# Optimization experiments

Measured on AMD Instinct MI355X. Metric: run time of the kernel, lower is better.

## Reference

```python
import jax, jax.numpy as jnp
import numpy as np

D = 1024
H = 16
HD = D // H  # 64
BASE = 10000.0


def _rope_tables(seq_len, dtype=jnp.float32):
    # inv_freq over even dims, rotate-half convention: emb = cat(freqs, freqs)
    inv_freq = 1.0 / (BASE ** (jnp.arange(0, HD, 2, dtype=jnp.float32) / HD))
    t = jnp.arange(seq_len, dtype=jnp.float32)
    freqs = jnp.einsum('i,j->ij', t, inv_freq)          # [S, HD/2]
    emb = jnp.concatenate([freqs, freqs], axis=-1)       # [S, HD]
    return jnp.cos(emb).astype(dtype), jnp.sin(emb).astype(dtype)


def _rotate_half(x):
    x1, x2 = jnp.split(x, 2, axis=-1)
    return jnp.concatenate([-x2, x1], axis=-1)


def setup_inputs() -> dict:
    key = jax.random.key(0)
    ks = jax.random.split(key, 5)
    B, S = 2, 2048
    scale = 0.02
    return {
        'x': jax.random.normal(ks[0], (B, S, D), dtype=jnp.float32),
        'wq': jax.random.normal(ks[1], (D, D), dtype=jnp.float32) * scale,
        'wk': jax.random.normal(ks[2], (D, D), dtype=jnp.float32) * scale,
        'wv': jax.random.normal(ks[3], (D, D), dtype=jnp.float32) * scale,
        'wo': jax.random.normal(ks[4], (D, D), dtype=jnp.float32) * scale,
    }


def reference(x, wq, wk, wv, wo):
    B, S, _ = x.shape
    # QKV projections (torch Linear: x @ W^T), split into heads -> [B, H, S, HD]
    def proj(w):
        return jnp.einsum('bsd,ed->bse', x, w).reshape(B, S, H, HD).transpose(0, 2, 1, 3)
    q, k, v = proj(wq), proj(wk), proj(wv)

    # RoPE (rotate-half)
    cos, sin = _rope_tables(S, x.dtype)                  # [S, HD]
    cos = cos[None, None, :, :]
    sin = sin[None, None, :, :]
    q = q * cos + _rotate_half(q) * sin
    k = k * cos + _rotate_half(k) * sin

    # causal scaled-dot-product attention
    scores = jnp.einsum('bhqd,bhkd->bhqk', q, k) / jnp.sqrt(jnp.array(HD, x.dtype))
    causal = jnp.tril(jnp.ones((S, S), dtype=bool))
    scores = jnp.where(causal[None, None], scores, jnp.finfo(x.dtype).min)
    attn = jax.nn.softmax(scores, axis=-1)
    out = jnp.einsum('bhqk,bhkd->bhqd', attn, v)         # [B, H, S, HD]

    out = out.transpose(0, 2, 1, 3).reshape(B, S, D)
    return jnp.einsum('bsd,ed->bse', out, wo)
```

## Files before the change

kernel.cpp:

```cpp
#include <hip/hip_runtime.h>
#include <cstdint>
#include <cstddef>

typedef unsigned short u16;
typedef unsigned int u32;
typedef __bf16 bf16x8 __attribute__((ext_vector_type(8)));
typedef float f32x4 __attribute__((ext_vector_type(4)));
typedef u16 u16x8 __attribute__((ext_vector_type(8)));
typedef u16 u16x4 __attribute__((ext_vector_type(4)));

#define DD 1024
#define HH 16
#define HDIM 64
#define BB 2
#define SS 2048
#define NQT 32

__device__ __forceinline__ u16 cvt(float f) {
  __bf16 h = (__bf16)f;
  return __builtin_bit_cast(u16, h);
}
__device__ __forceinline__ f32x4 mfma16(bf16x8 a, bf16x8 b, f32x4 c) {
  return __builtin_amdgcn_mfma_f32_16x16x32_bf16(a, b, c, 0, 0, 0);
}
__device__ __forceinline__ bf16x8 ld_bf8(const u16* p) {
  return __builtin_bit_cast(bf16x8, *(const u16x8*)p);
}
__device__ __forceinline__ void async16(const void* g, void* l) {
  __builtin_amdgcn_global_load_lds(
      (__attribute__((address_space(1))) void*)(uintptr_t)g,
      (__attribute__((address_space(3))) void*)l, 16, 0, 0);
}

__global__ void cast_all(const float* __restrict__ x, const float* __restrict__ wq,
                         const float* __restrict__ wk, const float* __restrict__ wv,
                         const float* __restrict__ wo, u16* __restrict__ xb,
                         u16* __restrict__ wqb, u16* __restrict__ wkb,
                         u16* __restrict__ wvb, u16* __restrict__ wob) {
  int i = blockIdx.x * 256 + threadIdx.x;
  const float* src;
  u16* dst;
  int off;
  if (i < (1 << 20)) {
    src = x; dst = xb; off = i;
  } else {
    int j = i - (1 << 20);
    int w = j >> 18;
    off = j & ((1 << 18) - 1);
    src = (w == 0) ? wq : (w == 1) ? wk : (w == 2) ? wv : wo;
    dst = (w == 0) ? wqb : (w == 1) ? wkb : (w == 2) ? wvb : wob;
  }
  float4 v = ((const float4*)src)[off];
  u16x4 o;
  o[0] = cvt(v.x); o[1] = cvt(v.y); o[2] = cvt(v.z); o[3] = cvt(v.w);
  *(u16x4*)&dst[(size_t)off * 4] = o;
}

__global__ __launch_bounds__(256) void gemm_qkv(
    const u16* __restrict__ xb, const u16* __restrict__ wq,
    const u16* __restrict__ wk, const u16* __restrict__ wv,
    u16* __restrict__ Qo, u16* __restrict__ Ko, u16* __restrict__ Vto) {
  __shared__ __align__(16) u16 As[2][128 * 32];
  __shared__ __align__(16) u16 Bs[2][128 * 32];
  const int t = threadIdx.x;
  const int w = t >> 6, l = t & 63, lane16 = l & 15, quad = l >> 4;
  const int m0 = blockIdx.x * 128, n0 = blockIdx.y * 128;
  const u16* wsel = (blockIdx.z == 0) ? wq : (blockIdx.z == 1) ? wk : wv;
  const int m_w = (w >> 1) * 64, n_w = (w & 1) * 64;
  const int srow = t >> 2, scol = (t & 3) * 8;
  const u16* a0 = &xb[(size_t)(m0 + srow) * DD + scol];
  const u16* a1 = &xb[(size_t)(m0 + 64 + srow) * DD + scol];
  const u16* b0 = &wsel[(size_t)(n0 + srow) * DD + scol];
  const u16* b1 = &wsel[(size_t)(n0 + 64 + srow) * DD + scol];

  async16(a0, &As[0][t * 8]);  async16(a1, &As[0][2048 + t * 8]);
  async16(b0, &Bs[0][t * 8]);  async16(b1, &Bs[0][2048 + t * 8]);

  f32x4 acc[4][4] = {};
  for (int kt = 0; kt < 32; ++kt) {
    __syncthreads();
    if (kt < 31) {
      const int nb = (kt + 1) & 1, ko = (kt + 1) * 32;
      async16(a0 + ko, &As[nb][t * 8]);
      async16(a1 + ko, &As[nb][2048 + t * 8]);
      async16(b0 + ko, &Bs[nb][t * 8]);
      async16(b1 + ko, &Bs[nb][2048 + t * 8]);
    }
    const u16* Ac = As[kt & 1];
    const u16* Bc = Bs[kt & 1];
    bf16x8 af[4], bfr[4];
#pragma unroll
    for (int mi = 0; mi < 4; ++mi)
      af[mi] = ld_bf8(&Ac[(m_w + mi * 16 + lane16) * 32 + quad * 8]);
#pragma unroll
    for (int ni = 0; ni < 4; ++ni)
      bfr[ni] = ld_bf8(&Bc[(n_w + ni * 16 + lane16) * 32 + quad * 8]);
#pragma unroll
    for (int mi = 0; mi < 4; ++mi)
#pragma unroll
      for (int ni = 0; ni < 4; ++ni)
        acc[mi][ni] = mfma16(af[mi], bfr[ni], acc[mi][ni]);
  }
  if (blockIdx.z == 2) {
#pragma unroll
    for (int mi = 0; mi < 4; ++mi) {
      int mbase = m0 + m_w + mi * 16 + quad * 4;
      int b = mbase >> 11, s0 = mbase & (SS - 1);
#pragma unroll
      for (int ni = 0; ni < 4; ++ni) {
        int e = n0 + n_w + ni * 16 + lane16;
        int h = e >> 6, d = e & 63;
        u16x4 pk;
#pragma unroll
        for (int r = 0; r < 4; ++r) pk[r] = cvt(acc[mi][ni][r]);
        *(u16x4*)&Vto[((size_t)(b * HH + h) * HDIM + d) * SS + s0] = pk;
      }
    }
  } else {
    u16* osel = (blockIdx.z == 0) ? Qo : Ko;
    const float scale = (blockIdx.z == 0) ? 0.18033688f : 1.0f;
    float invf[2];
    invf[0] = exp2f((float)lane16 * -0.4152410119f) * 0.15915494309f;
    invf[1] = exp2f((float)(16 + lane16) * -0.4152410119f) * 0.15915494309f;
    const int h = (n0 + n_w) >> 6;
#pragma unroll
    for (int mi = 0; mi < 4; ++mi) {
#pragma unroll
      for (int r = 0; r < 4; ++r) {
        int mrow = m0 + m_w + mi * 16 + quad * 4 + r;
        int b = mrow >> 11, s = mrow & (SS - 1);
        size_t rowbase = ((size_t)(b * HH + h) * SS + s) * HDIM;
#pragma unroll
        for (int ni = 0; ni < 2; ++ni) {
          float x1 = acc[mi][ni][r], x2 = acc[mi][ni + 2][r];
          float rv = (float)s * invf[ni];
          rv = rv - floorf(rv);
          float sn = __builtin_amdgcn_sinf(rv);
          float c  = __builtin_amdgcn_cosf(rv);
          int d = ni * 16 + lane16;
          osel[rowbase + d]      = cvt((x1 * c - x2 * sn) * scale);
          osel[rowbase + d + 32] = cvt((x2 * c + x1 * sn) * scale);
        }
      }
    }
  }
}

__global__ __launch_bounds__(256, 4) void attn_k(const u16* __restrict__ Qb,
                                                 const u16* __restrict__ Kb,
                                                 const u16* __restrict__ Vt,
                                                 u16* __restrict__ AO) {
  __shared__ __align__(16) u16 KsF[2][64 * 64];
  __shared__ __align__(16) u16 VtL[2][64 * 64];
  __shared__ __align__(16) u16 Ps[4][16 * 64];
  const int t = threadIdx.x;
  const int w = t >> 6, l = t & 63, lane16 = l & 15, quad = l >> 4;
  const int bh = blockIdx.x;
  const int jj = NQT - 1 - (int)blockIdx.y;
  const size_t base = (size_t)bh * SS * HDIM;
  const u16* Qp = Qb + base;
  const int b = bh >> 4, h = bh & 15;

  const int q0 = jj * 64;
  const int qrow = q0 + w * 16 + lane16;
  bf16x8 qf0 = ld_bf8(&Qp[(size_t)qrow * 64 + quad * 8]);
  bf16x8 qf1 = ld_bf8(&Qp[(size_t)qrow * 64 + 32 + quad * 8]);

  u16x8 onesu;
#pragma unroll
  for (int i = 0; i < 8; ++i) onesu[i] = 0x3F80;
  const bf16x8 ones = __builtin_bit_cast(bf16x8, onesu);

  f32x4 o[4] = {};
  f32x4 lacc = {};
  const f32x4 zf = {};

  const u16* kptr[2];
  const u16* vptr[2];
#pragma unroll
  for (int i = 0; i < 2; ++i) {
    int p = i * 256 + t;
    int r = p >> 3;
    int c = (p & 7) ^ (r & 7);
    kptr[i] = Kb + base + (size_t)r * 64 + c * 8;
    int d = p >> 3;
    int q = (p & 7) ^ (d & 7);
    vptr[i] = Vt + base + (size_t)d * SS + q * 8;
  }

#pragma unroll
  for (int i = 0; i < 2; ++i) {
    async16(kptr[i], &KsF[0][(i * 256 + t) * 8]);
    kptr[i] += 64 * 64;
    async16(vptr[i], &VtL[0][(i * 256 + t) * 8]);
    vptr[i] += 64;
  }

  u16* Pw = Ps[w];
  const int ktmax = jj;
  for (int kt = 0; kt <= ktmax; ++kt) {
    __syncthreads();
    if (kt < ktmax) {
      const int nb = (kt + 1) & 1;
#pragma unroll
      for (int i = 0; i < 2; ++i) {
        async16(kptr[i], &KsF[nb][(i * 256 + t) * 8]);
        kptr[i] += 64 * 64;
        async16(vptr[i], &VtL[nb][(i * 256 + t) * 8]);
        vptr[i] += 64;
      }
    }
    const u16* Kc = KsF[kt & 1];
    const u16* Vc = VtL[kt & 1];
    const int kv0 = kt * 64;
    f32x4 st[4];
    __builtin_amdgcn_s_setprio(1);
#pragma unroll
    for (int nc = 0; nc < 4; ++nc) {
      int rr = nc * 16 + lane16;
      int p0 = rr * 8 + (quad ^ (rr & 7));
      int p1 = rr * 8 + ((4 + quad) ^ (rr & 7));
      f32x4 a = mfma16(ld_bf8(&Kc[p0 * 8]), qf0, zf);
      a = mfma16(ld_bf8(&Kc[p1 * 8]), qf1, a);
      st[nc] = a;
    }
    __builtin_amdgcn_s_setprio(0);
    if (kt == ktmax) {
#pragma unroll
      for (int nc = 0; nc < 4; ++nc) {
        int kvb = kv0 + nc * 16 + quad * 4;
#pragma unroll
        for (int r = 0; r < 4; ++r)
          if (kvb + r > qrow) st[nc][r] = -3.0e38f;
      }
    }
#pragma unroll
    for (int nc = 0; nc < 4; ++nc)
#pragma unroll
      for (int r = 0; r < 4; ++r) st[nc][r] = __builtin_amdgcn_exp2f(st[nc][r]);
#pragma unroll
    for (int nc = 0; nc < 4; ++nc) {
      u16x4 pk;
#pragma unroll
      for (int r = 0; r < 4; ++r) pk[r] = cvt(st[nc][r]);
      int addr = lane16 * 64 + (((nc * 2 + (quad >> 1)) ^ (lane16 & 7)) * 8) + (quad & 1) * 4;
      *(u16x4*)&Pw[addr] = pk;
    }
    __builtin_amdgcn_s_setprio(1);
#pragma unroll
    for (int G = 0; G < 2; ++G) {
      int gc = ((G * 4 + quad) ^ (lane16 & 7)) * 8;
      bf16x8 pf = ld_bf8(&Pw[lane16 * 64 + gc]);
      lacc = mfma16(ones, pf, lacc);
#pragma unroll
      for (int nd = 0; nd < 4; ++nd) {
        int d = nd * 16 + lane16;
        bf16x8 bv = ld_bf8(&Vc[(size_t)d * 64 + gc]);
        o[nd] = mfma16(bv, pf, o[nd]);
      }
    }
    __builtin_amdgcn_s_setprio(0);
  }
  const float inv = 1.0f / lacc[0];
  const size_t rowb = (size_t)(b * SS + qrow) * DD + h * HDIM + quad * 4;
#pragma unroll
  for (int nd = 0; nd < 4; ++nd) {
    u16x4 pk;
#pragma unroll
    for (int r = 0; r < 4; ++r) pk[r] = cvt(o[nd][r] * inv);
    *(u16x4*)&AO[rowb + nd * 16] = pk;
  }
}

__global__ __launch_bounds__(256) void gemm_out(const u16* __restrict__ A, const u16* __restrict__ W,
                                                float* __restrict__ out) {
  __shared__ __align__(16) u16 As[2][128 * 32];
  __shared__ __align__(16) u16 Bs[2][64 * 32];
  const int t = threadIdx.x;
  const int w = t >> 6, l = t & 63, lane16 = l & 15, quad = l >> 4;
  const int m0 = blockIdx.x * 128, n0 = blockIdx.y * 64;
  const int m_w = (w >> 1) * 64, n_w = (w & 1) * 32;
  const int srow = t >> 2, scol = (t & 3) * 8;
  const u16* a0 = &A[(size_t)(m0 + srow) * DD + scol];
  const u16* a1 = &A[(size_t)(m0 + 64 + srow) * DD + scol];
  const u16* b0 = &W[(size_t)(n0 + srow) * DD + scol];

  async16(a0, &As[0][t * 8]);  async16(a1, &As[0][2048 + t * 8]);
  async16(b0, &Bs[0][t * 8]);

  f32x4 acc[4][2] = {};
  for (int kt = 0; kt < 32; ++kt) {
    __syncthreads();
    if (kt < 31) {
      const int nb = (kt + 1) & 1, ko = (kt + 1) * 32;
      async16(a0 + ko, &As[nb][t * 8]);
      async16(a1 + ko, &As[nb][2048 + t * 8]);
      async16(b0 + ko, &Bs[nb][t * 8]);
    }
    const u16* Ac = As[kt & 1];
    const u16* Bc = Bs[kt & 1];
    bf16x8 af[4], bfr[2];
#pragma unroll
    for (int mi = 0; mi < 4; ++mi)
      af[mi] = ld_bf8(&Ac[(m_w + mi * 16 + lane16) * 32 + quad * 8]);
#pragma unroll
    for (int ni = 0; ni < 2; ++ni)
      bfr[ni] = ld_bf8(&Bc[(n_w + ni * 16 + lane16) * 32 + quad * 8]);
#pragma unroll
    for (int mi = 0; mi < 4; ++mi)
#pragma unroll
      for (int ni = 0; ni < 2; ++ni)
        acc[mi][ni] = mfma16(af[mi], bfr[ni], acc[mi][ni]);
  }
#pragma unroll
  for (int mi = 0; mi < 4; ++mi) {
#pragma unroll
    for (int r = 0; r < 4; ++r) {
      int mrow = m0 + m_w + mi * 16 + quad * 4 + r;
#pragma unroll
      for (int ni = 0; ni < 2; ++ni) {
        int e = n0 + n_w + ni * 16 + lane16;
        out[(size_t)mrow * DD + e] = acc[mi][ni][r];
      }
    }
  }
}

extern "C" void kernel_launch(void* const* d_in, const int* in_sizes, int n_in,
                              void* d_out, int out_size, void* d_ws, size_t ws_size,
                              hipStream_t stream) {
  const float* x  = (const float*)d_in[0];
  const float* wq = (const float*)d_in[1];
  const float* wk = (const float*)d_in[2];
  const float* wv = (const float*)d_in[3];
  const float* wo = (const float*)d_in[4];
  float* out = (float*)d_out;
  char* ws = (char*)d_ws;

  u16* xb  = (u16*)(ws + (size_t)0);
  u16* wqb = (u16*)(ws + ((size_t)8  << 20));
  u16* wkb = (u16*)(ws + ((size_t)10 << 20));
  u16* wvb = (u16*)(ws + ((size_t)12 << 20));
  u16* wob = (u16*)(ws + ((size_t)14 << 20));
  u16* Qb  = (u16*)(ws + ((size_t)16 << 20));
  u16* Kb  = (u16*)(ws + ((size_t)24 << 20));
  u16* Vtg = (u16*)(ws + ((size_t)32 << 20));
  u16* AO  = (u16*)(ws + ((size_t)40 << 20));

  cast_all<<<8192, 256, 0, stream>>>(x, wq, wk, wv, wo, xb, wqb, wkb, wvb, wob);
  gemm_qkv<<<dim3(32, 8, 3), 256, 0, stream>>>(xb, wqb, wkb, wvb, Qb, Kb, Vtg);
  attn_k<<<dim3(32, 32), 256, 0, stream>>>(Qb, Kb, Vtg, AO);
  gemm_out<<<dim3(32, 16), 256, 0, stream>>>(AO, wob, out);
}
```

Baseline: 174.8 us.

## Triple-buffer LDS staging in projection GEMMs with explicit vmcnt waits

Both the QKV and output projection GEMMs move from double to triple-buffered LDS staging. Tiles are prefetched two steps ahead, and each step waits with an explicit partial s_waitcnt vmcnt before a raw s_barrier, instead of a full __syncthreads. The goal is to keep more global loads in flight and avoid draining all outstanding loads every iteration. The cost is more LDS per block, which may lower occupancy, and correctness now depends on the vmcnt counts matching the number of async loads issued per stage.

Measured after the change: 174.4 us. No clear change (-0.3%).

```diff
diff --git a/kernel.cpp b/kernel.cpp
--- a/kernel.cpp
+++ b/kernel.cpp
@@ -60,8 +60,8 @@
     const u16* __restrict__ xb, const u16* __restrict__ wq,
     const u16* __restrict__ wk, const u16* __restrict__ wv,
     u16* __restrict__ Qo, u16* __restrict__ Ko, u16* __restrict__ Vto) {
-  __shared__ __align__(16) u16 As[2][128 * 32];
-  __shared__ __align__(16) u16 Bs[2][128 * 32];
+  __shared__ __align__(16) u16 As[3 * 4096];
+  __shared__ __align__(16) u16 Bs[3 * 4096];
   const int t = threadIdx.x;
   const int w = t >> 6, l = t & 63, lane16 = l & 15, quad = l >> 4;
   const int m0 = blockIdx.x * 128, n0 = blockIdx.y * 128;
@@ -73,33 +73,42 @@
   const u16* b0 = &wsel[(size_t)(n0 + srow) * DD + scol];
   const u16* b1 = &wsel[(size_t)(n0 + 64 + srow) * DD + scol];
 
-  async16(a0, &As[0][t * 8]);  async16(a1, &As[0][2048 + t * 8]);
-  async16(b0, &Bs[0][t * 8]);  async16(b1, &Bs[0][2048 + t * 8]);
+  u16 *aC = As, *aN1 = As + 4096, *aN2 = As + 8192;
+  u16 *bC = Bs, *bN1 = Bs + 4096, *bN2 = Bs + 8192;
+
+  async16(a0, &aC[t * 8]);        async16(a1, &aC[2048 + t * 8]);
+  async16(b0, &bC[t * 8]);        async16(b1, &bC[2048 + t * 8]);
+  async16(a0 + 32, &aN1[t * 8]);  async16(a1 + 32, &aN1[2048 + t * 8]);
+  async16(b0 + 32, &bN1[t * 8]);  async16(b1 + 32, &bN1[2048 + t * 8]);
 
   f32x4 acc[4][4] = {};
   for (int kt = 0; kt < 32; ++kt) {
-    __syncthreads();
-    if (kt < 31) {
-      const int nb = (kt + 1) & 1, ko = (kt + 1) * 32;
-      async16(a0 + ko, &As[nb][t * 8]);
-      async16(a1 + ko, &As[nb][2048 + t * 8]);
-      async16(b0 + ko, &Bs[nb][t * 8]);
-      async16(b1 + ko, &Bs[nb][2048 + t * 8]);
-    }
-    const u16* Ac = As[kt & 1];
-    const u16* Bc = Bs[kt & 1];
+    if (kt < 31) asm volatile("s_waitcnt vmcnt(4)" ::: "memory");
+    else         asm volatile("s_waitcnt vmcnt(0)" ::: "memory");
+    __builtin_amdgcn_sched_barrier(0);
+    __builtin_amdgcn_s_barrier();
+    __builtin_amdgcn_sched_barrier(0);
+    if (kt < 30) {
+      const int ko = (kt + 2) * 32;
+      async16(a0 + ko, &aN2[t * 8]);
+      async16(a1 + ko, &aN2[2048 + t * 8]);
+      async16(b0 + ko, &bN2[t * 8]);
+      async16(b1 + ko, &bN2[2048 + t * 8]);
+    }
     bf16x8 af[4], bfr[4];
 #pragma unroll
     for (int mi = 0; mi < 4; ++mi)
-      af[mi] = ld_bf8(&Ac[(m_w + mi * 16 + lane16) * 32 + quad * 8]);
+      af[mi] = ld_bf8(&aC[(m_w + mi * 16 + lane16) * 32 + quad * 8]);
 #pragma unroll
     for (int ni = 0; ni < 4; ++ni)
-      bfr[ni] = ld_bf8(&Bc[(n_w + ni * 16 + lane16) * 32 + quad * 8]);
+      bfr[ni] = ld_bf8(&bC[(n_w + ni * 16 + lane16) * 32 + quad * 8]);
 #pragma unroll
     for (int mi = 0; mi < 4; ++mi)
 #pragma unroll
       for (int ni = 0; ni < 4; ++ni)
         acc[mi][ni] = mfma16(af[mi], bfr[ni], acc[mi][ni]);
+    u16* tp = aC; aC = aN1; aN1 = aN2; aN2 = tp;
+    tp = bC; bC = bN1; bN1 = bN2; bN2 = tp;
   }
   if (blockIdx.z == 2) {
 #pragma unroll
@@ -274,8 +283,8 @@
 
 __global__ __launch_bounds__(256) void gemm_out(const u16* __restrict__ A, const u16* __restrict__ W,
                                                 float* __restrict__ out) {
-  __shared__ __align__(16) u16 As[2][128 * 32];
-  __shared__ __align__(16) u16 Bs[2][64 * 32];
+  __shared__ __align__(16) u16 As[3 * 4096];
+  __shared__ __align__(16) u16 Bs[3 * 2048];
   const int t = threadIdx.x;
   const int w = t >> 6, l = t & 63, lane16 = l & 15, quad = l >> 4;
   const int m0 = blockIdx.x * 128, n0 = blockIdx.y * 64;
@@ -285,32 +294,41 @@
   const u16* a1 = &A[(size_t)(m0 + 64 + srow) * DD + scol];
   const u16* b0 = &W[(size_t)(n0 + srow) * DD + scol];
 
-  async16(a0, &As[0][t * 8]);  async16(a1, &As[0][2048 + t * 8]);
-  async16(b0, &Bs[0][t * 8]);
+  u16 *aC = As, *aN1 = As + 4096, *aN2 = As + 8192;
+  u16 *bC = Bs, *bN1 = Bs + 2048, *bN2 = Bs + 4096;
+
+  async16(a0, &aC[t * 8]);        async16(a1, &aC[2048 + t * 8]);
+  async16(b0, &bC[t * 8]);
+  async16(a0 + 32, &aN1[t * 8]);  async16(a1 + 32, &aN1[2048 + t * 8]);
+  async16(b0 + 32, &bN1[t * 8]);
 
   f32x4 acc[4][2] = {};
   for (int kt = 0; kt < 32; ++kt) {
-    __syncthreads();
-    if (kt < 31) {
-      const int nb = (kt + 1) & 1, ko = (kt + 1) * 32;
-      async16(a0 + ko, &As[nb][t * 8]);
-      async16(a1 + ko, &As[nb][2048 + t * 8]);
-      async16(b0 + ko, &Bs[nb][t * 8]);
-    }
-    const u16* Ac = As[kt & 1];
-    const u16* Bc = Bs[kt & 1];
+    if (kt < 31) asm volatile("s_waitcnt vmcnt(3)" ::: "memory");
+    else         asm volatile("s_waitcnt vmcnt(0)" ::: "memory");
+    __builtin_amdgcn_sched_barrier(0);
+    __builtin_amdgcn_s_barrier();
+    __builtin_amdgcn_sched_barrier(0);
+    if (kt < 30) {
+      const int ko = (kt + 2) * 32;
+      async16(a0 + ko, &aN2[t * 8]);
+      async16(a1 + ko, &aN2[2048 + t * 8]);
+      async16(b0 + ko, &bN2[t * 8]);
+    }
     bf16x8 af[4], bfr[2];
 #pragma unroll
     for (int mi = 0; mi < 4; ++mi)
-      af[mi] = ld_bf8(&Ac[(m_w + mi * 16 + lane16) * 32 + quad * 8]);
+      af[mi] = ld_bf8(&aC[(m_w + mi * 16 + lane16) * 32 + quad * 8]);
 #pragma unroll
     for (int ni = 0; ni < 2; ++ni)
-      bfr[ni] = ld_bf8(&Bc[(n_w + ni * 16 + lane16) * 32 + quad * 8]);
+      bfr[ni] = ld_bf8(&bC[(n_w + ni * 16 + lane16) * 32 + quad * 8]);
 #pragma unroll
     for (int mi = 0; mi < 4; ++mi)
 #pragma unroll
       for (int ni = 0; ni < 2; ++ni)
         acc[mi][ni] = mfma16(af[mi], bfr[ni], acc[mi][ni]);
+    u16* tp = aC; aC = aN1; aN1 = aN2; aN2 = tp;
+    tp = bC; bC = bN1; bN1 = bN2; bN2 = tp;
   }
 #pragma unroll
   for (int mi = 0; mi < 4; ++mi) {
```
